# Kernel optimization log

Hardware: AMD Instinct MI355X
Metric: run time of the kernel (lower is better)

## Reference

```python
import jax, jax.numpy as jnp
import numpy as np
import math

DIM_V = 512

def setup_inputs() -> dict:
    key = jax.random.key(0)
    k1, k2, k3, k4, k5, k6 = jax.random.split(key, 6)
    B, C, N, M = 8, DIM_V, 4096, 1024
    pcd_up = jax.random.normal(k1, (B, C, N), dtype=jnp.float32)
    pcd_down = jax.random.normal(k2, (B, C, M), dtype=jnp.float32)
    s = 1.0 / math.sqrt(C)
    Wq = jax.random.normal(k3, (C, C), dtype=jnp.float32) * s
    Wk = jax.random.normal(k4, (C, C), dtype=jnp.float32) * s
    Wv = jax.random.normal(k5, (C, C), dtype=jnp.float32) * s
    Wskip = jax.random.normal(k6, (C, C), dtype=jnp.float32) * s
    return {"pcd_up": pcd_up, "pcd_down": pcd_down, "Wq": Wq, "Wk": Wk, "Wv": Wv, "Wskip": Wskip}

def reference(pcd_up, pcd_down, Wq, Wk, Wv, Wskip):
    # 1x1 Conv1d == per-point linear: weight [out_c, in_c]
    q = jnp.einsum('oc,bcn->bon', Wq, pcd_up)      # [B, C, N]
    k = jnp.einsum('oc,bcm->bom', Wk, pcd_down)    # [B, C, M]
    v = jnp.einsum('oc,bcm->bom', Wv, pcd_down)    # [B, C, M]
    C = q.shape[1]
    scale = jnp.sqrt(jnp.asarray(C, dtype=q.dtype))  # sqrt(q.shape[-2]) = sqrt(C)
    energy = jnp.einsum('bcn,bcm->bnm', q, k) / scale  # [B, N, M]
    attention = jax.nn.softmax(energy, axis=-1)
    x = jnp.einsum('bnm,bcm->bcn', attention, v)       # [B, C, N]
    skip = jnp.einsum('oc,bcn->bon', Wskip, pcd_up)
    return skip + x
```

## Files before the change

### kernel.cpp

```cpp
#include <hip/hip_runtime.h>
#include <cstddef>

#define Bn 8
#define Cd 512
#define Nn 4096
#define Mm 1024

typedef __attribute__((ext_vector_type(8))) short s8v;
typedef __attribute__((ext_vector_type(4))) float v4f;
typedef __attribute__((ext_vector_type(16))) float v16f;

__device__ __forceinline__ float b2f(unsigned short u) {
    union { unsigned int i; float f; } v; v.i = ((unsigned int)u) << 16; return v.f;
}
__device__ __forceinline__ unsigned short f2b(float f) {
    union { float f; unsigned int i; } v; v.f = f;
    unsigned int x = v.i;
    unsigned int r = (x + 0x7FFFu + ((x >> 16) & 1u)) >> 16;
    return (unsigned short)r;
}
__device__ __forceinline__ v4f mfma16(s8v a, s8v b, v4f c) {
    return __builtin_amdgcn_mfma_f32_16x16x32_bf16(a, b, c, 0, 0, 0);
}
__device__ __forceinline__ v16f mfma32(s8v a, s8v b, v16f c) {
    return __builtin_amdgcn_mfma_f32_32x32x16_bf16(a, b, c, 0, 0, 0);
}
__device__ __forceinline__ void gload_lds16(const unsigned short* gsrc, unsigned char* lds) {
    __builtin_amdgcn_global_load_lds(
        (const __attribute__((address_space(1))) unsigned int*)gsrc,
        (__attribute__((address_space(3))) unsigned int*)lds, 16, 0, 0);
}

__global__ __launch_bounds__(256) void convwf(const float* __restrict__ Wq, const float* __restrict__ Wk,
                                              const float* __restrict__ Wv, const float* __restrict__ Ws,
                                              unsigned short* __restrict__ Wf) {
    const float* S = (blockIdx.y == 0) ? Wq : (blockIdx.y == 1) ? Wk : (blockIdx.y == 2) ? Wv : Ws;
    const int o16 = blockIdx.x;
    const int t = threadIdx.x;
    const int l = t & 63, sub = t >> 6;
    const int lq = l & 15, quad = l >> 4;
    unsigned short* dst = Wf + (size_t)blockIdx.y * 262144;
#pragma unroll
    for (int rep = 0; rep < 4; ++rep) {
        int cstep = sub * 4 + rep;
        const float* src = S + (size_t)(o16 * 16 + lq) * Cd + cstep * 32 + quad * 8;
        float4 va = *(const float4*)(src);
        float4 vb = *(const float4*)(src + 4);
        union { ushort4 h[2]; uint4 q; } pk;
        pk.h[0].x = f2b(va.x); pk.h[0].y = f2b(va.y); pk.h[0].z = f2b(va.z); pk.h[0].w = f2b(va.w);
        pk.h[1].x = f2b(vb.x); pk.h[1].y = f2b(vb.y); pk.h[1].z = f2b(vb.z); pk.h[1].w = f2b(vb.w);
        *(uint4*)(dst + ((size_t)(o16 * 16 + cstep) * 64 + l) * 8) = pk.q;
    }
}

__global__ __launch_bounds__(256) void convx(const float* __restrict__ X,
                                             unsigned short* __restrict__ Xt,
                                             int Nx) {
    __shared__ float Lf[64][65];
    const int t = threadIdx.x;
    const int b = blockIdx.z, c0 = blockIdx.y * 64;
    const int nl0 = blockIdx.x * 64;
    const int cl = t >> 4, n4 = (t & 15) * 4;
    const float* Xb = X + (size_t)b * Cd * Nx + nl0;
#pragma unroll
    for (int cc = 0; cc < 4; ++cc) {
        int c = cc * 16 + cl;
        float4 v = *(const float4*)(Xb + (size_t)(c0 + c) * Nx + n4);
        Lf[n4 + 0][c] = v.x; Lf[n4 + 1][c] = v.y;
        Lf[n4 + 2][c] = v.z; Lf[n4 + 3][c] = v.w;
    }
    __syncthreads();
    unsigned short* Xtb = Xt + ((size_t)b * Nx + nl0) * Cd + c0;
#pragma unroll
    for (int rep = 0; rep < 2; ++rep) {
        int u = t + rep * 256;
        int n = u >> 3, c8 = (u & 7) * 8;
        union { ushort4 h[2]; uint4 q; } pk;
        pk.h[0].x = f2b(Lf[n][c8 + 0]); pk.h[0].y = f2b(Lf[n][c8 + 1]);
        pk.h[0].z = f2b(Lf[n][c8 + 2]); pk.h[0].w = f2b(Lf[n][c8 + 3]);
        pk.h[1].x = f2b(Lf[n][c8 + 4]); pk.h[1].y = f2b(Lf[n][c8 + 5]);
        pk.h[1].z = f2b(Lf[n][c8 + 6]); pk.h[1].w = f2b(Lf[n][c8 + 7]);
        *(uint4*)(Xtb + (size_t)n * Cd + c8) = pk.q;
    }
}

template <int PAIRB>
__global__ __launch_bounds__(256, 2) void gemm4(const unsigned short* __restrict__ Wf,
                                                unsigned short* XY,
                                                unsigned short* __restrict__ Y2,
                                                float* __restrict__ outF,
                                                int Nc) {
    __shared__ __align__(16) unsigned char raw[8192];
    const int t = threadIdx.x;
    const int l = t & 63, w = t >> 6, lq = t & 15, quad = (t >> 4) & 3;
    const int bid = blockIdx.x;
    const int b = bid & 7, n0 = (bid >> 3) * 32;
    unsigned short* Xb = XY + ((size_t)b * Nc + n0) * Cd;
    const unsigned short* W1f = Wf + (size_t)1 * 262144 + (size_t)l * 8;
    const unsigned short* W2f = Wf + (size_t)2 * 262144 + (size_t)l * 8;

    v4f acc1[8][2], acc2[8][2];
#pragma unroll
    for (int i = 0; i < 8; ++i)
#pragma unroll
        for (int nt = 0; nt < 2; ++nt) {
            acc1[i][nt] = (v4f){0.f, 0.f, 0.f, 0.f};
            acc2[i][nt] = (v4f){0.f, 0.f, 0.f, 0.f};
        }

#define STAGE4(s, c0)                                                            \
    if (t < 128) gload_lds16(Xb + (size_t)(t >> 2) * Cd + (c0) + (t & 3) * 8,    \
                             raw + (s) * 2048 + t * 16);

    STAGE4(0, 0);
    for (int step = 0; step < 16; ++step) {
        const int c0 = step * 32, cur = step & 1;
        __syncthreads();
        s8v a1[8], a2[8];
#pragma unroll
        for (int i = 0; i < 8; ++i)
            a1[i] = *(const s8v*)(W1f + ((size_t)((w * 8 + i) * 16 + step) << 9));
#pragma unroll
        for (int i = 0; i < 8; ++i)
            a2[i] = *(const s8v*)(W2f + ((size_t)((w * 8 + i) * 16 + step) << 9));
        if (step < 15) { STAGE4(cur ^ 1, c0 + 32) }
        const short* Xs = (const short*)(raw + cur * 2048);
        s8v bf0 = *(const s8v*)(Xs + lq * 32 + quad * 8);
        s8v bf1 = *(const s8v*)(Xs + (lq + 16) * 32 + quad * 8);
#pragma unroll
        for (int i = 0; i < 8; ++i) {
            acc1[i][0] = mfma16(a1[i], bf0, acc1[i][0]);
            acc1[i][1] = mfma16(a1[i], bf1, acc1[i][1]);
        }
#pragma unroll
        for (int i = 0; i < 8; ++i) {
            acc2[i][0] = mfma16(a2[i], bf0, acc2[i][0]);
            acc2[i][1] = mfma16(a2[i], bf1, acc2[i][1]);
        }
    }
#undef STAGE4
    __syncthreads();

    const int half = quad >> 1, ebase = (quad & 1) * 4;
    {
        unsigned short* Kb = XY + (size_t)b * Mm * Cd;
        const int mt = n0 >> 5;
#pragma unroll
        for (int i = 0; i < 8; ++i) {
            int kb = w * 8 + i;
#pragma unroll
            for (int nt = 0; nt < 2; ++nt) {
                int lf = (nt * 16 + lq) + 32 * half;
                ushort4 v;
                v.x = f2b(acc1[i][nt][0]); v.y = f2b(acc1[i][nt][1]);
                v.z = f2b(acc1[i][nt][2]); v.w = f2b(acc1[i][nt][3]);
                *(ushort4*)(Kb + ((size_t)(mt * 32 + kb) * 64 + lf) * 8 + ebase) = v;
            }
        }
    }
    short (*Vst)[40] = reinterpret_cast<short(*)[40]>(raw + w * 1280);
    unsigned short* Vb0 = Y2 + (size_t)b * Cd * Mm;
#pragma unroll
    for (int i = 0; i < 8; ++i) {
#pragma unroll
        for (int nt = 0; nt < 2; ++nt)
#pragma unroll
            for (int r = 0; r < 4; ++r)
                Vst[quad * 4 + r][nt * 16 + lq] = (short)f2b(acc2[i][nt][r]);
        int c_abs = (w * 8 + i) * 16 + (l >> 2);
        int m8 = l & 3;
        int ct = c_abs >> 5, mb = (n0 >> 4) + (m8 >> 1);
        int lf = (c_abs & 31) + 32 * (m8 & 1);
        uint4 v = *(const uint4*)(&Vst[l >> 2][m8 * 8]);
        *(uint4*)(Vb0 + ((size_t)(ct * 64 + mb) * 64 + lf) * 8) = v;
    }
}

template <int MODE>
__global__ __launch_bounds__(256) void gemm_mfma(const float* __restrict__ W,
                                                 const float* __restrict__ X,
                                                 float* __restrict__ Yf,
                                                 unsigned short* __restrict__ Yb,
                                                 int Nx) {
    __shared__ short Xs[64][40];
    __shared__ short Tt[16][72];
    const int t = threadIdx.x;
    const int w = t >> 6, lq = t & 15, quad = (t >> 4) & 3;
    const int b = blockIdx.z, o0 = blockIdx.y * 64, n0 = blockIdx.x * 64;
    const float* Xb = X + (size_t)b * Cd * Nx;
    const float* Wrow = W + (size_t)(o0 + w * 16 + lq) * Cd;

    v4f acc[4];
#pragma unroll
    for (int i = 0; i < 4; ++i) acc[i] = (v4f){0.f, 0.f, 0.f, 0.f};

    for (int c0 = 0; c0 < Cd; c0 += 32) {
#pragma unroll
        for (int p = 0; p < 2; ++p) {
            int i = t + p * 256;
            int c = i >> 4;
            int n4 = (i & 15) * 4;
            float4 x = *(const float4*)(Xb + (size_t)(c0 + c) * Nx + n0 + n4);
            Xs[n4 + 0][c] = (short)f2b(x.x); Xs[n4 + 1][c] = (short)f2b(x.y);
            Xs[n4 + 2][c] = (short)f2b(x.z); Xs[n4 + 3][c] = (short)f2b(x.w);
        }
        union { unsigned short h[8]; s8v s; } af;
        {
            float4 wa = *(const float4*)(Wrow + c0 + quad * 8);
            float4 wb = *(const float4*)(Wrow + c0 + quad * 8 + 4);
            af.h[0] = f2b(wa.x); af.h[1] = f2b(wa.y); af.h[2] = f2b(wa.z); af.h[3] = f2b(wa.w);
            af.h[4] = f2b(wb.x); af.h[5] = f2b(wb.y); af.h[6] = f2b(wb.z); af.h[7] = f2b(wb.w);
        }
        __syncthreads();
#pragma unroll
        for (int nt = 0; nt < 4; ++nt) {
            s8v bf = *(const s8v*)(&Xs[nt * 16 + lq][quad * 8]);
            acc[nt] = mfma16(af.s, bf, acc[nt]);
        }
        __syncthreads();
    }

    if (MODE == 0) {
#pragma unroll
        for (int nt = 0; nt < 4; ++nt)
#pragma unroll
            for (int r = 0; r < 4; ++r) {
                int o = o0 + w * 16 + quad * 4 + r;
                int n = n0 + nt * 16 + lq;
                Yf[((size_t)b * Cd + o) * Nx + n] = acc[nt][r];
            }
    } else {
#pragma unroll
        for (int nt = 0; nt < 4; ++nt) {
#pragma unroll
            for (int r = 0; r < 4; ++r)
                Tt[lq][w * 16 + quad * 4 + r] = (short)f2b(acc[nt][r]);
            __syncthreads();
            int nrow = t >> 4, o4 = (t & 15) * 4;
            ushort4 val = *(const ushort4*)(&Tt[nrow][o4]);
            *(ushort4*)(Yb + ((size_t)b * Nx + n0 + nt * 16 + nrow) * Cd + o0 + o4) = val;
            __syncthreads();
        }
    }
}

__global__ __launch_bounds__(512, 2) void attn_f(const float* __restrict__ up,
                                                 const unsigned short* __restrict__ Wf,
                                                 const unsigned short* __restrict__ Kf,
                                                 const unsigned short* __restrict__ Vf,
                                                 float* __restrict__ out) {
    __shared__ __align__(16) unsigned char Ls[104192];
    unsigned char* Lq = Ls;
    unsigned short* Pb = (unsigned short*)(Ls + 65536);
    float* pmaxS  = (float*)(Ls + 99328);
    float* psumS  = (float*)(Ls + 101376);
    float* muS    = (float*)(Ls + 103424);
    float* ssumS  = (float*)(Ls + 103680);
    float* alphaS = (float*)(Ls + 103936);
    float* OtA    = (float*)Ls;

    const int t = threadIdx.x;
    const int l = t & 63, w = t >> 6;
    const int lcol = l & 31, lhalf = l >> 5;
    const int lq = l & 15, quad = (l >> 4) & 3;
    const int bid = blockIdx.x;
    const int b = bid & 7, n0 = (bid >> 3) * 64;

    {
        const float* ub = up + (size_t)b * Cd * Nn + n0;
#pragma unroll
        for (int it = 0; it < 16; ++it) {
            int i = it * 512 + t;
            int c = i >> 4, n4 = (i & 15) * 4;
            float4 v = *(const float4*)(ub + (size_t)c * Nn + n4);
            int cu = c >> 3, ce = (c & 7) * 2;
            float vv[4] = {v.x, v.y, v.z, v.w};
#pragma unroll
            for (int j = 0; j < 4; ++j) {
                int n = n4 + j;
                *(unsigned short*)(Lq + ((n * 64 + (cu ^ (n & 15))) << 4) + ce) = f2b(vv[j]);
            }
        }
    }
    __syncthreads();

    {
        v4f aq[4][4], ask[4][4];
#pragma unroll
        for (int oi = 0; oi < 4; ++oi)
#pragma unroll
            for (int ni = 0; ni < 4; ++ni) {
                aq[oi][ni] = (v4f){0.f, 0.f, 0.f, 0.f};
                ask[oi][ni] = (v4f){0.f, 0.f, 0.f, 0.f};
            }
        const unsigned short* WqF = Wf + (size_t)l * 8;
        const unsigned short* WsF = Wf + (size_t)3 * 262144 + (size_t)l * 8;
        for (int step = 0; step < 16; ++step) {
            s8v a1[4], a2[4];
#pragma unroll
            for (int oi = 0; oi < 4; ++oi)
                a1[oi] = *(const s8v*)(WqF + ((size_t)((w * 4 + oi) * 16 + step) << 9));
#pragma unroll
            for (int oi = 0; oi < 4; ++oi)
                a2[oi] = *(const s8v*)(WsF + ((size_t)((w * 4 + oi) * 16 + step) << 9));
#pragma unroll
            for (int ni = 0; ni < 4; ++ni) {
                int n = ni * 16 + lq;
                s8v bf = *(const s8v*)(Lq + ((n * 64 + ((step * 4 + quad) ^ lq)) << 4));
#pragma unroll
                for (int oi = 0; oi < 4; ++oi) {
                    aq[oi][ni] = mfma16(a1[oi], bf, aq[oi][ni]);
                    ask[oi][ni] = mfma16(a2[oi], bf, ask[oi][ni]);
                }
            }
        }
#pragma unroll
        for (int oi = 0; oi < 4; ++oi)
#pragma unroll
            for (int ni = 0; ni < 4; ++ni)
#pragma unroll
                for (int r = 0; r < 4; ++r) {
                    int o = w * 64 + oi * 16 + quad * 4 + r;
                    int n = n0 + ni * 16 + lq;
                    out[((size_t)b * Cd + o) * Nn + n] = ask[oi][ni][r];
                }
        __syncthreads();
#pragma unroll
        for (int oi = 0; oi < 4; ++oi)
#pragma unroll
            for (int ni = 0; ni < 4; ++ni) {
                int n = ni * 16 + lq;
                int cu = w * 8 + oi * 2 + (quad >> 1);
                ushort4 pk;
                pk.x = f2b(aq[oi][ni][0]); pk.y = f2b(aq[oi][ni][1]);
                pk.z = f2b(aq[oi][ni][2]); pk.w = f2b(aq[oi][ni][3]);
                *(ushort4*)(Lq + ((n * 64 + (cu ^ lq)) << 4) + (quad & 1) * 8) = pk;
            }
    }
    if (t < 64) { muS[t] = -1e30f; ssumS[t] = 0.f; }

    v16f o_acc[2][2];
#pragma unroll
    for (int nh = 0; nh < 2; ++nh)
#pragma unroll
        for (int ti = 0; ti < 2; ++ti)
#pragma unroll
            for (int r = 0; r < 16; ++r) o_acc[nh][ti][r] = 0.f;
    __syncthreads();

    const unsigned short* Kfb = Kf + (size_t)b * Mm * Cd + (size_t)l * 8;
    const unsigned short* Vfb = Vf + (size_t)b * Cd * Mm + (size_t)l * 8;
    const int q0 = lcol * 64, q1 = (lcol + 32) * 64;
    const int swz = lcol & 15;
    const float sc = 0.04419417382415922f;

    for (int m0 = 0; m0 < Mm; m0 += 256) {
        v16f st0, st1;
#pragma unroll
        for (int r = 0; r < 16; ++r) { st0[r] = 0.f; st1[r] = 0.f; }
        const unsigned short* kp = Kfb + (size_t)(((m0 >> 5) + w) * 32) * 512;
#pragma unroll
        for (int kb8 = 0; kb8 < 4; ++kb8) {
            uint4 ka[8];
#pragma unroll
            for (int j = 0; j < 8; ++j) ka[j] = *(const uint4*)(kp + (size_t)(kb8 * 8 + j) * 512);
            __builtin_amdgcn_s_setprio(1);
#pragma unroll
            for (int j = 0; j < 8; ++j) {
                int kb = kb8 * 8 + j;
                int uo = (kb * 2 + lhalf) ^ swz;
                s8v qf0 = *(const s8v*)(Lq + ((q0 + uo) << 4));
                s8v qf1 = *(const s8v*)(Lq + ((q1 + uo) << 4));
                union { uint4 u; s8v s; } av; av.u = ka[j];
                st0 = mfma32(av.s, qf0, st0);
                st1 = mfma32(av.s, qf1, st1);
            }
            __builtin_amdgcn_s_setprio(0);
        }
        uint4 v0p[8];
        {
            const unsigned short* vc = Vfb + (size_t)((w * 2) * 64 + (m0 >> 4)) * 512;
#pragma unroll
            for (int j = 0; j < 8; ++j) v0p[j] = *(const uint4*)(vc + (size_t)j * 512);
        }
#pragma unroll
        for (int r = 0; r < 16; ++r) { st0[r] *= sc; st1[r] *= sc; }
        float tm0 = st0[0], tm1 = st1[0];
#pragma unroll
        for (int r = 1; r < 16; ++r) { tm0 = fmaxf(tm0, st0[r]); tm1 = fmaxf(tm1, st1[r]); }
        tm0 = fmaxf(tm0, __shfl_xor(tm0, 32));
        tm1 = fmaxf(tm1, __shfl_xor(tm1, 32));
        if (l < 32) {
            pmaxS[l * 8 + w] = tm0;
            pmaxS[(l + 32) * 8 + w] = tm1;
        }
        __syncthreads();
        {
            int row = t >> 3, p = t & 7;
            float v = pmaxS[row * 8 + p];
            v = fmaxf(v, __shfl_xor(v, 1));
            v = fmaxf(v, __shfl_xor(v, 2));
            v = fmaxf(v, __shfl_xor(v, 4));
            if (p == 0) {
                float mold = muS[row];
                float mx = fmaxf(mold, v);
                alphaS[row] = __expf(mold - mx);
                muS[row] = mx;
            }
        }
        __syncthreads();
        {
            float mx0 = muS[lcol], mx1 = muS[lcol + 32];
            float e0[16], e1[16], rs0 = 0.f, rs1 = 0.f;
#pragma unroll
            for (int r = 0; r < 16; ++r) {
                e0[r] = __expf(st0[r] - mx0); rs0 += e0[r];
                e1[r] = __expf(st1[r] - mx1); rs1 += e1[r];
            }
            rs0 += __shfl_xor(rs0, 32);
            rs1 += __shfl_xor(rs1, 32);
            if (l < 32) {
                psumS[l * 8 + w] = rs0;
                psumS[(l + 32) * 8 + w] = rs1;
            }
#pragma unroll
            for (int rg = 0; rg < 4; ++rg) {
                ushort4 pk0, pk1;
                pk0.x = f2b(e0[rg * 4 + 0]); pk0.y = f2b(e0[rg * 4 + 1]);
                pk0.z = f2b(e0[rg * 4 + 2]); pk0.w = f2b(e0[rg * 4 + 3]);
                pk1.x = f2b(e1[rg * 4 + 0]); pk1.y = f2b(e1[rg * 4 + 1]);
                pk1.z = f2b(e1[rg * 4 + 2]); pk1.w = f2b(e1[rg * 4 + 3]);
                *(ushort4*)(Pb + lcol * 264 + w * 32 + 8 * rg + 4 * lhalf) = pk0;
                *(ushort4*)(Pb + (lcol + 32) * 264 + w * 32 + 8 * rg + 4 * lhalf) = pk1;
            }
        }
        __syncthreads();
        {
            int row = t >> 3, p = t & 7;
            float v = psumS[row * 8 + p];
            v += __shfl_xor(v, 1);
            v += __shfl_xor(v, 2);
            v += __shfl_xor(v, 4);
            if (p == 0) ssumS[row] = ssumS[row] * alphaS[row] + v;
        }

        float ar0[16], ar1[16];
#pragma unroll
        for (int r = 0; r < 16; ++r) {
            int crow = (r & 3) + 8 * (r >> 2) + 4 * lhalf;
            ar0[r] = alphaS[crow];
            ar1[r] = alphaS[32 + crow];
        }
#pragma unroll
        for (int ti = 0; ti < 2; ++ti)
#pragma unroll
            for (int r = 0; r < 16; ++r) {
                o_acc[0][ti][r] *= ar0[r];
                o_acc[1][ti][r] *= ar1[r];
            }

#pragma unroll
        for (int h = 0; h < 2; ++h) {
            s8v pA0[8], pA1[8];
#pragma unroll
            for (int j = 0; j < 8; ++j) {
                pA0[j] = *(const s8v*)(Pb + lcol * 264 + (h * 8 + j) * 16 + lhalf * 8);
                pA1[j] = *(const s8v*)(Pb + (lcol + 32) * 264 + (h * 8 + j) * 16 + lhalf * 8);
            }
#pragma unroll
            for (int ti = 0; ti < 2; ++ti) {
                uint4 vb[8];
                if (h == 0 && ti == 0) {
#pragma unroll
                    for (int j = 0; j < 8; ++j) vb[j] = v0p[j];
                } else {
                    const unsigned short* vc = Vfb + (size_t)((w * 2 + ti) * 64 + (m0 >> 4) + h * 8) * 512;
#pragma unroll
                    for (int j = 0; j < 8; ++j) vb[j] = *(const uint4*)(vc + (size_t)j * 512);
                }
                __builtin_amdgcn_s_setprio(1);
#pragma unroll
                for (int j = 0; j < 8; ++j) {
                    union { uint4 u; s8v s; } bv; bv.u = vb[j];
                    o_acc[0][ti] = mfma32(pA0[j], bv.s, o_acc[0][ti]);
                    o_acc[1][ti] = mfma32(pA1[j], bv.s, o_acc[1][ti]);
                }
                __builtin_amdgcn_s_setprio(0);
            }
        }
        __syncthreads();
    }

    float inv0[16], inv1[16];
#pragma unroll
    for (int r = 0; r < 16; ++r) {
        int crow = (r & 3) + 8 * (r >> 2) + 4 * lhalf;
        inv0[r] = 1.0f / ssumS[crow];
        inv1[r] = 1.0f / ssumS[32 + crow];
    }
    float* OtW = OtA + w * 32 * 36;
#pragma unroll
    for (int nh = 0; nh < 2; ++nh)
#pragma unroll
        for (int ti = 0; ti < 2; ++ti) {
#pragma unroll
            for (int r = 0; r < 16; ++r) {
                int crow = (r & 3) + 8 * (r >> 2) + 4 * lhalf;
                OtW[lcol * 36 + crow] = o_acc[nh][ti][r] * (nh ? inv1[r] : inv0[r]);
            }
            int cloc = l >> 1, half = l & 1;
            int cabs = (w * 2 + ti) * 32 + cloc;
            const float* src = OtW + cloc * 36 + half * 16;
            float* op = out + ((size_t)b * Cd + cabs) * Nn + n0 + nh * 32 + half * 16;
#pragma unroll
            for (int j = 0; j < 4; ++j) {
                float4 a = *(const float4*)(src + j * 4);
                float4 g = *(const float4*)(op + j * 4);
                g.x += a.x; g.y += a.y; g.z += a.z; g.w += a.w;
                *(float4*)(op + j * 4) = g;
            }
        }
}

__device__ __forceinline__ float u2lo(unsigned int u) {
    union { unsigned int i; float f; } v; v.i = u << 16; return v.f;
}
__device__ __forceinline__ float u2hi(unsigned int u) {
    union { unsigned int i; float f; } v; v.i = u & 0xFFFF0000u; return v.f;
}

__global__ __launch_bounds__(256) void attn_k(const float* __restrict__ up,
                                              const float* __restrict__ Wq,
                                              const unsigned short* __restrict__ Ktb,
                                              const unsigned short* __restrict__ Vtb,
                                              float* __restrict__ out) {
    __shared__ float Qs[16][516];
    __shared__ __align__(16) unsigned char Sraw[24576];
    unsigned short (*Us)[16]  = reinterpret_cast<unsigned short(*)[16]>(Sraw);
    unsigned short (*Wt)[512] = reinterpret_cast<unsigned short(*)[512]>(Sraw + 16384);
    float (*Ps)[65] = reinterpret_cast<float(*)[65]>(Sraw);
    float* mu_s     = reinterpret_cast<float*>(Sraw + 4160);
    float* ssum_s   = reinterpret_cast<float*>(Sraw + 4224);
    float* alpha_s  = reinterpret_cast<float*>(Sraw + 4288);

    const int t = threadIdx.x;
    const int b = blockIdx.y;
    const int n0 = blockIdx.x * 16;
    const int row = t & 15;
    const int grp = t >> 4;

    for (int i = t; i < Cd * 16; i += 256) {
        int c = i >> 4, r = i & 15;
        Us[c][r] = f2b(up[((size_t)b * Cd + c) * Nn + n0 + r]);
    }
    __syncthreads();

    float acc[32];
#pragma unroll
    for (int j = 0; j < 32; ++j) acc[j] = 0.f;

    for (int k0 = 0; k0 < Cd; k0 += 8) {
        for (int i = t; i < 1024; i += 256) {
            int oc = i >> 1;
            int kc = (i & 1) * 4;
            float4 wv = *(const float4*)(Wq + (size_t)oc * Cd + k0 + kc);
            Wt[kc + 0][oc] = f2b(wv.x); Wt[kc + 1][oc] = f2b(wv.y);
            Wt[kc + 2][oc] = f2b(wv.z); Wt[kc + 3][oc] = f2b(wv.w);
        }
        __syncthreads();
#pragma unroll
        for (int k = 0; k < 8; ++k) {
            float u = b2f(Us[k0 + k][row]);
            const ushort4* wr = (const ushort4*)(&Wt[k][grp * 32]);
#pragma unroll
            for (int j4 = 0; j4 < 8; ++j4) {
                ushort4 wv = wr[j4];
                acc[j4 * 4 + 0] += u * b2f(wv.x);
                acc[j4 * 4 + 1] += u * b2f(wv.y);
                acc[j4 * 4 + 2] += u * b2f(wv.z);
                acc[j4 * 4 + 3] += u * b2f(wv.w);
            }
        }
        __syncthreads();
    }

    const float scale = 0.04419417382415922f;
#pragma unroll
    for (int j = 0; j < 32; ++j) Qs[row][grp * 32 + j] = acc[j] * scale;
    if (t < 16) { mu_s[t] = -1e30f; ssum_s[t] = 0.f; }
#pragma unroll
    for (int j = 0; j < 32; ++j) acc[j] = 0.f;
    __syncthreads();

    const float4* qr = (const float4*)(&Qs[row][0]);

    for (int m0 = 0; m0 < Mm; m0 += 64) {
        {
            int mb = m0 + grp * 4;
            const uint4* K0 = (const uint4*)(Ktb + ((size_t)b * Mm + mb + 0) * Cd);
            const uint4* K1 = (const uint4*)(Ktb + ((size_t)b * Mm + mb + 1) * Cd);
            const uint4* K2 = (const uint4*)(Ktb + ((size_t)b * Mm + mb + 2) * Cd);
            const uint4* K3 = (const uint4*)(Ktb + ((size_t)b * Mm + mb + 3) * Cd);
            float a0 = 0.f, a1 = 0.f, a2 = 0.f, a3 = 0.f;
#pragma unroll 4
            for (int c8 = 0; c8 < Cd / 8; ++c8) {
                float4 qa = qr[2 * c8], qb = qr[2 * c8 + 1];
                uint4 k0v = K0[c8], k1v = K1[c8], k2v = K2[c8], k3v = K3[c8];
                a0 += qa.x * u2lo(k0v.x) + qa.y * u2hi(k0v.x) + qa.z * u2lo(k0v.y) + qa.w * u2hi(k0v.y)
                    + qb.x * u2lo(k0v.z) + qb.y * u2hi(k0v.z) + qb.z * u2lo(k0v.w) + qb.w * u2hi(k0v.w);
                a1 += qa.x * u2lo(k1v.x) + qa.y * u2hi(k1v.x) + qa.z * u2lo(k1v.y) + qa.w * u2hi(k1v.y)
                    + qb.x * u2lo(k1v.z) + qb.y * u2hi(k1v.z) + qb.z * u2lo(k1v.w) + qb.w * u2hi(k1v.w);
                a2 += qa.x * u2lo(k2v.x) + qa.y * u2hi(k2v.x) + qa.z * u2lo(k2v.y) + qa.w * u2hi(k2v.y)
                    + qb.x * u2lo(k2v.z) + qb.y * u2hi(k2v.z) + qb.z * u2lo(k2v.w) + qb.w * u2hi(k2v.w);
                a3 += qa.x * u2lo(k3v.x) + qa.y * u2hi(k3v.x) + qa.z * u2lo(k3v.y) + qa.w * u2hi(k3v.y)
                    + qb.x * u2lo(k3v.z) + qb.y * u2hi(k3v.z) + qb.z * u2lo(k3v.w) + qb.w * u2hi(k3v.w);
            }
            Ps[row][grp * 4 + 0] = a0;
            Ps[row][grp * 4 + 1] = a1;
            Ps[row][grp * 4 + 2] = a2;
            Ps[row][grp * 4 + 3] = a3;
        }
        __syncthreads();
        if (t < 16) {
            float mold = mu_s[t];
            float mx = mold;
            for (int m = 0; m < 64; ++m) mx = fmaxf(mx, Ps[t][m]);
            float al = __expf(mold - mx);
            float s = ssum_s[t] * al;
            for (int m = 0; m < 64; ++m) {
                float p = __expf(Ps[t][m] - mx);
                Ps[t][m] = p;
                s += p;
            }
            mu_s[t] = mx; ssum_s[t] = s; alpha_s[t] = al;
        }
        __syncthreads();
        {
            float arr = alpha_s[row];
#pragma unroll
            for (int j = 0; j < 32; ++j) acc[j] *= arr;
            const unsigned short* Vbase = Vtb + (size_t)b * Mm * Cd + (size_t)grp * 32;
            for (int m = 0; m < 64; ++m) {
                float p = Ps[row][m];
                const uint4* vr = (const uint4*)(Vbase + (size_t)(m0 + m) * Cd);
#pragma unroll
                for (int j4 = 0; j4 < 4; ++j4) {
                    uint4 v = vr[j4];
                    acc[j4 * 8 + 0] += p * u2lo(v.x); acc[j4 * 8 + 1] += p * u2hi(v.x);
                    acc[j4 * 8 + 2] += p * u2lo(v.y); acc[j4 * 8 + 3] += p * u2hi(v.y);
                    acc[j4 * 8 + 4] += p * u2lo(v.z); acc[j4 * 8 + 5] += p * u2hi(v.z);
                    acc[j4 * 8 + 6] += p * u2lo(v.w); acc[j4 * 8 + 7] += p * u2hi(v.w);
                }
            }
        }
        __syncthreads();
    }

    float invv = 1.0f / ssum_s[row];
#pragma unroll
    for (int j = 0; j < 32; ++j) {
        int c = grp * 32 + j;
        size_t idx = ((size_t)b * Cd + c) * Nn + n0 + row;
        out[idx] = out[idx] + acc[j] * invv;
    }
}

extern "C" void kernel_launch(void* const* d_in, const int* in_sizes, int n_in,
                              void* d_out, int out_size, void* d_ws, size_t ws_size,
                              hipStream_t stream) {
    const float* up   = (const float*)d_in[0];
    const float* down = (const float*)d_in[1];
    const float* Wq   = (const float*)d_in[2];
    const float* Wk   = (const float*)d_in[3];
    const float* Wv   = (const float*)d_in[4];
    const float* Wsk  = (const float*)d_in[5];
    float* out = (float*)d_out;

    const size_t szK = (size_t)Bn * Mm * Cd;
    const size_t szW = (size_t)4 * Cd * Cd;

    if (ws_size >= (2 * szK + szW) * 2) {
        unsigned short* XK = (unsigned short*)d_ws;
        unsigned short* Vf = XK + szK;
        unsigned short* Wf = Vf + szK;
        convwf<<<dim3(32, 4), 256, 0, stream>>>(Wq, Wk, Wv, Wsk, Wf);
        convx<<<dim3(Mm / 64, Cd / 64, Bn), 256, 0, stream>>>(down, XK, Mm);
        gemm4<0><<<dim3(Bn * (Mm / 32)), 256, 0, stream>>>(Wf, XK, Vf, nullptr, Mm);
        attn_f<<<dim3((Nn / 64) * Bn), 512, 0, stream>>>(up, Wf, XK, Vf, out);
    } else {
        unsigned short* Ktb = (unsigned short*)d_ws;
        unsigned short* Vtb = Ktb + szK;
        gemm_mfma<2><<<dim3(Mm / 64, Cd / 64, Bn), 256, 0, stream>>>(Wk, down, nullptr, Ktb, Mm);
        gemm_mfma<2><<<dim3(Mm / 64, Cd / 64, Bn), 256, 0, stream>>>(Wv, down, nullptr, Vtb, Mm);
        gemm_mfma<0><<<dim3(Nn / 64, Cd / 64, Bn), 256, 0, stream>>>(Wsk, up, out, nullptr, Nn);
        attn_k<<<dim3(Nn / 16, Bn), 256, 0, stream>>>(up, Wq, Ktb, Vtb, out);
    }
}
```

Before: 281.4 us.

## Fuse down conversion into KV GEMM and keep skip result in registers

Removes the separate convx transpose kernel: gemm_kv now loads fp32 pcd_down directly, converts pairs to bf16 into a swizzled LDS tile and computes K and V, split across twice as many blocks by output half. In attn_f the skip GEMM accumulators stay in registers and are added in LDS before a single store, replacing the global skip write followed by a read-modify-write. The up-tile load is also packed two channels per 32-bit LDS store. This cuts one launch and several global round trips, at the cost of more live registers in attn_f and larger LDS in gemm_kv.

```diff
diff --git a/kernel.cpp b/kernel.cpp
--- a/kernel.cpp
+++ b/kernel.cpp
@@ -19,16 +19,14 @@
     unsigned int r = (x + 0x7FFFu + ((x >> 16) & 1u)) >> 16;
     return (unsigned short)r;
 }
+__device__ __forceinline__ unsigned int f2b2(float lo, float hi) {
+    return (unsigned int)f2b(lo) | ((unsigned int)f2b(hi) << 16);
+}
 __device__ __forceinline__ v4f mfma16(s8v a, s8v b, v4f c) {
     return __builtin_amdgcn_mfma_f32_16x16x32_bf16(a, b, c, 0, 0, 0);
 }
 __device__ __forceinline__ v16f mfma32(s8v a, s8v b, v16f c) {
     return __builtin_amdgcn_mfma_f32_32x32x16_bf16(a, b, c, 0, 0, 0);
-}
-__device__ __forceinline__ void gload_lds16(const unsigned short* gsrc, unsigned char* lds) {
-    __builtin_amdgcn_global_load_lds(
-        (const __attribute__((address_space(1))) unsigned int*)gsrc,
-        (__attribute__((address_space(3))) unsigned int*)lds, 16, 0, 0);
 }
 
 __global__ __launch_bounds__(256) void convwf(const float* __restrict__ Wq, const float* __restrict__ Wk,
@@ -53,104 +51,77 @@
     }
 }
 
-__global__ __launch_bounds__(256) void convx(const float* __restrict__ X,
-                                             unsigned short* __restrict__ Xt,
-                                             int Nx) {
-    __shared__ float Lf[64][65];
-    const int t = threadIdx.x;
-    const int b = blockIdx.z, c0 = blockIdx.y * 64;
-    const int nl0 = blockIdx.x * 64;
-    const int cl = t >> 4, n4 = (t & 15) * 4;
-    const float* Xb = X + (size_t)b * Cd * Nx + nl0;
-#pragma unroll
-    for (int cc = 0; cc < 4; ++cc) {
-        int c = cc * 16 + cl;
-        float4 v = *(const float4*)(Xb + (size_t)(c0 + c) * Nx + n4);
-        Lf[n4 + 0][c] = v.x; Lf[n4 + 1][c] = v.y;
-        Lf[n4 + 2][c] = v.z; Lf[n4 + 3][c] = v.w;
-    }
-    __syncthreads();
-    unsigned short* Xtb = Xt + ((size_t)b * Nx + nl0) * Cd + c0;
-#pragma unroll
-    for (int rep = 0; rep < 2; ++rep) {
-        int u = t + rep * 256;
-        int n = u >> 3, c8 = (u & 7) * 8;
-        union { ushort4 h[2]; uint4 q; } pk;
-        pk.h[0].x = f2b(Lf[n][c8 + 0]); pk.h[0].y = f2b(Lf[n][c8 + 1]);
-        pk.h[0].z = f2b(Lf[n][c8 + 2]); pk.h[0].w = f2b(Lf[n][c8 + 3]);
-        pk.h[1].x = f2b(Lf[n][c8 + 4]); pk.h[1].y = f2b(Lf[n][c8 + 5]);
-        pk.h[1].z = f2b(Lf[n][c8 + 6]); pk.h[1].w = f2b(Lf[n][c8 + 7]);
-        *(uint4*)(Xtb + (size_t)n * Cd + c8) = pk.q;
-    }
-}
-
-template <int PAIRB>
-__global__ __launch_bounds__(256, 2) void gemm4(const unsigned short* __restrict__ Wf,
-                                                unsigned short* XY,
-                                                unsigned short* __restrict__ Y2,
-                                                float* __restrict__ outF,
-                                                int Nc) {
-    __shared__ __align__(16) unsigned char raw[8192];
+__global__ __launch_bounds__(256, 2) void gemm_kv(const unsigned short* __restrict__ Wf,
+                                                  const float* __restrict__ down,
+                                                  unsigned short* __restrict__ Kf,
+                                                  unsigned short* __restrict__ Vf) {
+    __shared__ __align__(16) unsigned char raw[37888];
     const int t = threadIdx.x;
     const int l = t & 63, w = t >> 6, lq = t & 15, quad = (t >> 4) & 3;
     const int bid = blockIdx.x;
-    const int b = bid & 7, n0 = (bid >> 3) * 32;
-    unsigned short* Xb = XY + ((size_t)b * Nc + n0) * Cd;
+    const int b = bid & 7, mt = (bid >> 3) & 31, half = bid >> 8;
+    const int m0 = mt * 32;
+    const float* db = down + (size_t)b * Cd * Mm + m0;
     const unsigned short* W1f = Wf + (size_t)1 * 262144 + (size_t)l * 8;
     const unsigned short* W2f = Wf + (size_t)2 * 262144 + (size_t)l * 8;
 
-    v4f acc1[8][2], acc2[8][2];
-#pragma unroll
-    for (int i = 0; i < 8; ++i)
+    {
+#pragma unroll
+        for (int rep = 0; rep < 8; ++rep) {
+            int u = rep * 256 + t;
+            int c2 = u >> 3, m4 = (u & 7) * 4;
+            float4 a = *(const float4*)(db + (size_t)(2 * c2) * Mm + m4);
+            float4 c = *(const float4*)(db + (size_t)(2 * c2 + 1) * Mm + m4);
+            int cu = c2 >> 2, sb = (c2 & 3) * 4;
+            float av[4] = {a.x, a.y, a.z, a.w};
+            float cv[4] = {c.x, c.y, c.z, c.w};
+#pragma unroll
+            for (int j = 0; j < 4; ++j) {
+                int m = m4 + j;
+                *(unsigned int*)(raw + ((m * 64 + (cu ^ (m & 15))) << 4) + sb) = f2b2(av[j], cv[j]);
+            }
+        }
+    }
+    __syncthreads();
+
+    v4f acc1[4][2], acc2[4][2];
+#pragma unroll
+    for (int i = 0; i < 4; ++i)
 #pragma unroll
         for (int nt = 0; nt < 2; ++nt) {
             acc1[i][nt] = (v4f){0.f, 0.f, 0.f, 0.f};
             acc2[i][nt] = (v4f){0.f, 0.f, 0.f, 0.f};
         }
 
-#define STAGE4(s, c0)                                                            \
-    if (t < 128) gload_lds16(Xb + (size_t)(t >> 2) * Cd + (c0) + (t & 3) * 8,    \
-                             raw + (s) * 2048 + t * 16);
-
-    STAGE4(0, 0);
     for (int step = 0; step < 16; ++step) {
-        const int c0 = step * 32, cur = step & 1;
-        __syncthreads();
-        s8v a1[8], a2[8];
-#pragma unroll
-        for (int i = 0; i < 8; ++i)
-            a1[i] = *(const s8v*)(W1f + ((size_t)((w * 8 + i) * 16 + step) << 9));
-#pragma unroll
-        for (int i = 0; i < 8; ++i)
-            a2[i] = *(const s8v*)(W2f + ((size_t)((w * 8 + i) * 16 + step) << 9));
-        if (step < 15) { STAGE4(cur ^ 1, c0 + 32) }
-        const short* Xs = (const short*)(raw + cur * 2048);
-        s8v bf0 = *(const s8v*)(Xs + lq * 32 + quad * 8);
-        s8v bf1 = *(const s8v*)(Xs + (lq + 16) * 32 + quad * 8);
-#pragma unroll
-        for (int i = 0; i < 8; ++i) {
+        s8v a1[4], a2[4];
+#pragma unroll
+        for (int i = 0; i < 4; ++i) {
+            int o16 = half * 16 + w * 4 + i;
+            a1[i] = *(const s8v*)(W1f + ((size_t)(o16 * 16 + step) << 9));
+            a2[i] = *(const s8v*)(W2f + ((size_t)(o16 * 16 + step) << 9));
+        }
+        s8v bf0 = *(const s8v*)(raw + ((lq * 64 + ((step * 4 + quad) ^ lq)) << 4));
+        s8v bf1 = *(const s8v*)(raw + (((lq + 16) * 64 + ((step * 4 + quad) ^ lq)) << 4));
+#pragma unroll
+        for (int i = 0; i < 4; ++i) {
             acc1[i][0] = mfma16(a1[i], bf0, acc1[i][0]);
             acc1[i][1] = mfma16(a1[i], bf1, acc1[i][1]);
-        }
-#pragma unroll
-        for (int i = 0; i < 8; ++i) {
             acc2[i][0] = mfma16(a2[i], bf0, acc2[i][0]);
             acc2[i][1] = mfma16(a2[i], bf1, acc2[i][1]);
         }
     }
-#undef STAGE4
     __syncthreads();
 
-    const int half = quad >> 1, ebase = (quad & 1) * 4;
+    const int hq = quad >> 1, ebase = (quad & 1) * 4;
     {
-        unsigned short* Kb = XY + (size_t)b * Mm * Cd;
-        const int mt = n0 >> 5;
-#pragma unroll
-        for (int i = 0; i < 8; ++i) {
-            int kb = w * 8 + i;
+        unsigned short* Kb = Kf + (size_t)b * Mm * Cd;
+#pragma unroll
+        for (int i = 0; i < 4; ++i) {
+            int kb = half * 16 + w * 4 + i;
 #pragma unroll
             for (int nt = 0; nt < 2; ++nt) {
-                int lf = (nt * 16 + lq) + 32 * half;
+                int lf = (nt * 16 + lq) + 32 * hq;
                 ushort4 v;
                 v.x = f2b(acc1[i][nt][0]); v.y = f2b(acc1[i][nt][1]);
                 v.z = f2b(acc1[i][nt][2]); v.w = f2b(acc1[i][nt][3]);
@@ -158,18 +129,19 @@
             }
         }
     }
-    short (*Vst)[40] = reinterpret_cast<short(*)[40]>(raw + w * 1280);
-    unsigned short* Vb0 = Y2 + (size_t)b * Cd * Mm;
-#pragma unroll
-    for (int i = 0; i < 8; ++i) {
+    short (*Vst)[40] = reinterpret_cast<short(*)[40]>(raw + 32768 + w * 1280);
+    unsigned short* Vb0 = Vf + (size_t)b * Cd * Mm;
+#pragma unroll
+    for (int i = 0; i < 4; ++i) {
+        int o16 = half * 16 + w * 4 + i;
 #pragma unroll
         for (int nt = 0; nt < 2; ++nt)
 #pragma unroll
             for (int r = 0; r < 4; ++r)
                 Vst[quad * 4 + r][nt * 16 + lq] = (short)f2b(acc2[i][nt][r]);
-        int c_abs = (w * 8 + i) * 16 + (l >> 2);
+        int c_abs = o16 * 16 + (l >> 2);
         int m8 = l & 3;
-        int ct = c_abs >> 5, mb = (n0 >> 4) + (m8 >> 1);
+        int ct = c_abs >> 5, mb = (m0 >> 4) + (m8 >> 1);
         int lf = (c_abs & 31) + 32 * (m8 & 1);
         uint4 v = *(const uint4*)(&Vst[l >> 2][m8 * 8]);
         *(uint4*)(Vb0 + ((size_t)(ct * 64 + mb) * 64 + lf) * 8) = v;
@@ -266,26 +238,30 @@
     const int bid = blockIdx.x;
     const int b = bid & 7, n0 = (bid >> 3) * 64;
 
+    v4f ask[4][4];
+
     {
         const float* ub = up + (size_t)b * Cd * Nn + n0;
 #pragma unroll
-        for (int it = 0; it < 16; ++it) {
-            int i = it * 512 + t;
-            int c = i >> 4, n4 = (i & 15) * 4;
-            float4 v = *(const float4*)(ub + (size_t)c * Nn + n4);
-            int cu = c >> 3, ce = (c & 7) * 2;
-            float vv[4] = {v.x, v.y, v.z, v.w};
+        for (int it = 0; it < 8; ++it) {
+            int u = it * 512 + t;
+            int c2 = u >> 4, n4 = (u & 15) * 4;
+            float4 a = *(const float4*)(ub + (size_t)(2 * c2) * Nn + n4);
+            float4 c = *(const float4*)(ub + (size_t)(2 * c2 + 1) * Nn + n4);
+            int cu = c2 >> 2, sb = (c2 & 3) * 4;
+            float av[4] = {a.x, a.y, a.z, a.w};
+            float cv[4] = {c.x, c.y, c.z, c.w};
 #pragma unroll
             for (int j = 0; j < 4; ++j) {
                 int n = n4 + j;
-                *(unsigned short*)(Lq + ((n * 64 + (cu ^ (n & 15))) << 4) + ce) = f2b(vv[j]);
+                *(unsigned int*)(Lq + ((n * 64 + (cu ^ (n & 15))) << 4) + sb) = f2b2(av[j], cv[j]);
             }
         }
     }
     __syncthreads();
 
     {
-        v4f aq[4][4], ask[4][4];
+        v4f aq[4][4];
 #pragma unroll
         for (int oi = 0; oi < 4; ++oi)
 #pragma unroll
@@ -314,16 +290,6 @@
                 }
             }
         }
-#pragma unroll
-        for (int oi = 0; oi < 4; ++oi)
-#pragma unroll
-            for (int ni = 0; ni < 4; ++ni)
-#pragma unroll
-                for (int r = 0; r < 4; ++r) {
-                    int o = w * 64 + oi * 16 + quad * 4 + r;
-                    int n = n0 + ni * 16 + lq;
-                    out[((size_t)b * Cd + o) * Nn + n] = ask[oi][ni][r];
-                }
         __syncthreads();
 #pragma unroll
         for (int oi = 0; oi < 4; ++oi)
@@ -508,17 +474,25 @@
                 int crow = (r & 3) + 8 * (r >> 2) + 4 * lhalf;
                 OtW[lcol * 36 + crow] = o_acc[nh][ti][r] * (nh ? inv1[r] : inv0[r]);
             }
+#pragma unroll
+            for (int oi2 = 0; oi2 < 2; ++oi2)
+#pragma unroll
+                for (int ni2 = 0; ni2 < 2; ++ni2) {
+                    int oi = ti * 2 + oi2, ni = nh * 2 + ni2;
+#pragma unroll
+                    for (int r = 0; r < 4; ++r) {
+                        int cloc2 = oi2 * 16 + quad * 4 + r;
+                        int nloc = ni2 * 16 + lq;
+                        OtW[cloc2 * 36 + nloc] += ask[oi][ni][r];
+                    }
+                }
             int cloc = l >> 1, half = l & 1;
             int cabs = (w * 2 + ti) * 32 + cloc;
             const float* src = OtW + cloc * 36 + half * 16;
             float* op = out + ((size_t)b * Cd + cabs) * Nn + n0 + nh * 32 + half * 16;
 #pragma unroll
-            for (int j = 0; j < 4; ++j) {
-                float4 a = *(const float4*)(src + j * 4);
-                float4 g = *(const float4*)(op + j * 4);
-                g.x += a.x; g.y += a.y; g.z += a.z; g.w += a.w;
-                *(float4*)(op + j * 4) = g;
-            }
+            for (int j = 0; j < 4; ++j)
+                *(float4*)(op + j * 4) = *(const float4*)(src + j * 4);
         }
 }
 
@@ -680,13 +654,12 @@
     const size_t szW = (size_t)4 * Cd * Cd;
 
     if (ws_size >= (2 * szK + szW) * 2) {
-        unsigned short* XK = (unsigned short*)d_ws;
-        unsigned short* Vf = XK + szK;
+        unsigned short* Kf = (unsigned short*)d_ws;
+        unsigned short* Vf = Kf + szK;
         unsigned short* Wf = Vf + szK;
         convwf<<<dim3(32, 4), 256, 0, stream>>>(Wq, Wk, Wv, Wsk, Wf);
-        convx<<<dim3(Mm / 64, Cd / 64, Bn), 256, 0, stream>>>(down, XK, Mm);
-        gemm4<0><<<dim3(Bn * (Mm / 32)), 256, 0, stream>>>(Wf, XK, Vf, nullptr, Mm);
-        attn_f<<<dim3((Nn / 64) * Bn), 512, 0, stream>>>(up, Wf, XK, Vf, out);
+        gemm_kv<<<dim3(Bn * (Mm / 32) * 2), 256, 0, stream>>>(Wf, down, Kf, Vf);
+        attn_f<<<dim3((Nn / 64) * Bn), 512, 0, stream>>>(up, Wf, Kf, Vf, out);
     } else {
         unsigned short* Ktb = (unsigned short*)d_ws;
         unsigned short* Vtb = Ktb + szK;
```

After: 386.9 us. 1.38x slower.
